# Optimization experiments

Hardware: AMD Instinct MI355X
Metric: run time of the kernel (lower is better)

## Reference

```python
import jax, jax.numpy as jnp
import numpy as np

B, S, D, H = 2, 2048, 1024, 16
HD = D // H  # head_dim = 64


def setup_inputs() -> dict:
    key = jax.random.key(0)
    ks = jax.random.split(key, 5)
    scale = 0.02
    x = jax.random.normal(ks[0], (B, S, D), dtype=jnp.float32)
    Wq = scale * jax.random.normal(ks[1], (H, D, HD), dtype=jnp.float32)
    Wk = scale * jax.random.normal(ks[2], (H, D, HD), dtype=jnp.float32)
    Wv = scale * jax.random.normal(ks[3], (H, D, HD), dtype=jnp.float32)
    Wo = scale * jax.random.normal(ks[4], (D, D), dtype=jnp.float32)
    bq = jnp.zeros((H, HD), dtype=jnp.float32)
    bk = jnp.zeros((H, HD), dtype=jnp.float32)
    bv = jnp.zeros((H, HD), dtype=jnp.float32)
    bo = jnp.zeros((D,), dtype=jnp.float32)
    return {"x": x, "Wq": Wq, "bq": bq, "Wk": Wk, "bk": bk,
            "Wv": Wv, "bv": bv, "Wo": Wo, "bo": bo}


def reference(x, Wq, bq, Wk, bk, Wv, bv, Wo, bo):
    # Per-head QKV projections (the torch module's per-head nn.Linear list,
    # vectorized over the head axis h). Dropout is identity (eval mode).
    q = jnp.einsum("bsd,hde->bhse", x, Wq) + bq[None, :, None, :]  # [B,H,S,HD]
    k = jnp.einsum("bsd,hde->bhse", x, Wk) + bk[None, :, None, :]
    v = jnp.einsum("bsd,hde->bhse", x, Wv) + bv[None, :, None, :]

    norm = jnp.asarray(np.sqrt(HD), dtype=x.dtype)
    scores = jnp.einsum("bhse,bhte->bhst", q, k) / norm  # [B,H,S,S]
    causal = jnp.tril(jnp.ones((S, S), dtype=bool))
    scores = jnp.where(causal[None, None], scores, jnp.asarray(-jnp.inf, dtype=scores.dtype))
    attn = jax.nn.softmax(scores, axis=-1)

    wv = jnp.einsum("bhst,bhte->bhse", attn, v)          # [B,H,S,HD]
    wv = jnp.transpose(wv, (0, 2, 1, 3)).reshape(B, S, D)  # concat heads on last dim
    out = wv @ Wo.T + bo                                   # output projection
    return out
```

## Files before the change

kernel.cpp:

```cpp
#include <hip/hip_runtime.h>


#define DD 1024
#define SS 2048
#define BB 2
#define HH 16
#define HD 64
#define QSCALE 0.18033688011112042f
#define LSTR 88

typedef __attribute__((ext_vector_type(8))) short short8;
typedef __attribute__((ext_vector_type(4))) float float4v;
typedef unsigned short ushort;
typedef unsigned int uint;

__device__ inline ushort f2bf(float f) {
    union { float f; uint i; } v; v.f = f;
    uint r = v.i + 0x7FFF + ((v.i >> 16) & 1);
    return (ushort)(r >> 16);
}
__device__ inline ushort f2bf_f(float f) {
    union { float f; uint i; } v; v.f = f;
    return (ushort)((v.i + 0x8000u) >> 16);
}

__device__ __forceinline__ void cp16(const ushort* g, ushort* l) {
    __builtin_amdgcn_global_load_lds((const __attribute__((address_space(1))) void*)g,
                                     (__attribute__((address_space(3))) void*)l,
                                     16, 0, 0);
}

__global__ __launch_bounds__(256) void cvt_all(const float* __restrict__ x,
                                               const float* __restrict__ Wo,
                                               ushort* __restrict__ xb,
                                               ushort* __restrict__ Wob) {
    const int NX4 = (BB * SS * DD) / 4;
    int i = blockIdx.x * 256 + threadIdx.x;
    const float* src; ushort* dst; int j;
    if (i < NX4) { src = x; dst = xb; j = i; }
    else         { src = Wo; dst = Wob; j = i - NX4; }
    float4 v = ((const float4*)src)[j];
    ushort o[4] = { f2bf(v.x), f2bf(v.y), f2bf(v.z), f2bf(v.w) };
    ((uint2*)dst)[j] = *(const uint2*)o;
}

__global__ __launch_bounds__(256) void transpose_w3(const float* __restrict__ Wq,
                                                    const float* __restrict__ Wk,
                                                    const float* __restrict__ Wv,
                                                    ushort* __restrict__ W3T) {
    __shared__ ushort T[64][65];
    int z = blockIdx.z;
    const float* W = z == 0 ? Wq : (z == 1 ? Wk : Wv);
    int h = blockIdx.y, d0 = blockIdx.x * 64;
    const float* Wh = W + h * DD * HD;
    ushort* Wt = W3T + ((size_t)z * HH + h) * HD * DD;
    int t = threadIdx.x;
    #pragma unroll
    for (int i = 0; i < 4; i++) {
        int idx = t + i * 256;
        int d = idx >> 4, e4 = (idx & 15) * 4;
        float4 v = *(const float4*)(Wh + (d0 + d) * HD + e4);
        T[d][e4 + 0] = f2bf(v.x); T[d][e4 + 1] = f2bf(v.y);
        T[d][e4 + 2] = f2bf(v.z); T[d][e4 + 3] = f2bf(v.w);
    }
    __syncthreads();
    #pragma unroll
    for (int i = 0; i < 2; i++) {
        int idx = t + i * 256;
        int e = idx >> 3, d8 = (idx & 7) * 8;
        ushort tmp[8];
        #pragma unroll
        for (int j = 0; j < 8; j++) tmp[j] = T[d8 + j][e];
        *(uint4*)(Wt + e * DD + d0 + d8) = *(uint4*)tmp;
    }
}

__global__ __launch_bounds__(256) void gemm_qkv(const ushort* __restrict__ xb,
                                                const ushort* __restrict__ W3T,
                                                const float* __restrict__ bq,
                                                const float* __restrict__ bk,
                                                const float* __restrict__ bv,
                                                ushort* __restrict__ qb,
                                                ushort* __restrict__ kb,
                                                ushort* __restrict__ vT) {
    __shared__ ushort Al[128 * 32];
    __shared__ ushort Bl[128 * 32];
    int z = blockIdx.z;
    const ushort* Wt   = W3T + (size_t)z * HH * HD * DD;
    const float*  bias = z == 0 ? bq : (z == 1 ? bk : bv);
    int m0 = blockIdx.x * 128, n0 = blockIdx.y * 128;
    int t = threadIdx.x, lane = t & 63, w = t >> 6;
    int wm = w & 1, wn = w >> 1;
    int qm = lane >> 4, lm = lane & 15;

    float4v acc[4][4] = {};
    for (int k0 = 0; k0 < DD; k0 += 32) {
        __syncthreads();
        #pragma unroll
        for (int r2 = 0; r2 < 2; r2++) {
            int c = t + r2 * 256;
            cp16(xb + (size_t)(m0 + (c >> 2)) * DD + k0 + (c & 3) * 8, Al + c * 8);
            cp16(Wt + (size_t)(n0 + (c >> 2)) * DD + k0 + (c & 3) * 8, Bl + c * 8);
        }
        __syncthreads();
        short8 a[4], b[4];
        #pragma unroll
        for (int i = 0; i < 4; i++)
            a[i] = *(const short8*)(Al + (wm * 64 + i * 16 + lm) * 32 + qm * 8);
        #pragma unroll
        for (int j = 0; j < 4; j++)
            b[j] = *(const short8*)(Bl + (wn * 64 + j * 16 + lm) * 32 + qm * 8);
        #pragma unroll
        for (int i = 0; i < 4; i++)
            #pragma unroll
            for (int j = 0; j < 4; j++)
                acc[i][j] = __builtin_amdgcn_mfma_f32_16x16x32_bf16(a[i], b[j], acc[i][j], 0, 0, 0);
    }
    if (z == 2) {
        #pragma unroll
        for (int j = 0; j < 4; j++) {
            int n = n0 + wn * 64 + j * 16 + lm;
            int h = n >> 6, e = n & 63;
            float bb = bias[n];
            #pragma unroll
            for (int i = 0; i < 4; i++) {
                int m = m0 + wm * 64 + i * 16 + qm * 4;
                int b_ = m >> 11, s = m & (SS - 1);
                ushort p4[4];
                #pragma unroll
                for (int r = 0; r < 4; r++) p4[r] = f2bf_f(acc[i][j][r] + bb);
                *(uint2*)(vT + ((size_t)(b_ * HH + h) * HD + e) * SS + s) = *(const uint2*)p4;
            }
        }
    } else {
        ushort* Out = z == 0 ? qb : kb;
        float sc = z == 0 ? QSCALE : 1.0f;
        #pragma unroll
        for (int j = 0; j < 4; j++) {
            int n = n0 + wn * 64 + j * 16 + lm;
            float bb = bias[n];
            #pragma unroll
            for (int i = 0; i < 4; i++)
                #pragma unroll
                for (int r = 0; r < 4; r++) {
                    int m = m0 + wm * 64 + i * 16 + qm * 4 + r;
                    Out[(size_t)m * DD + n] = f2bf_f((acc[i][j][r] + bb) * sc);
                }
        }
    }
}

__global__ __launch_bounds__(512) void attn(const ushort* __restrict__ Q,
                                            const ushort* __restrict__ K,
                                            const ushort* __restrict__ VT,
                                            ushort* __restrict__ O) {
    __shared__ ushort Ql[128][LSTR];
    __shared__ ushort Kl[2][64][LSTR];
    __shared__ ushort Vl[2][64][LSTR];
    __shared__ ushort Pl[8][16][LSTR];
    int px = blockIdx.x, bh = blockIdx.y;
    int b = bh >> 4, h = bh & 15;
    const ushort* Qp = Q + (size_t)b * SS * DD + h * HD;
    const ushort* Kp = K + (size_t)b * SS * DD + h * HD;
    const ushort* Vp = VT + (size_t)bh * HD * SS;
    int t = threadIdx.x, lane = t & 63, w = t >> 6;
    int qm = lane >> 4, lm = lane & 15;
    int row0 = t >> 3, colc = (t & 7) * 8;

    #pragma unroll
    for (int ph = 0; ph < 2; ph++) {
        int qt = ph ? 15 - px : px;
        int m0 = qt * 128;
        int njt = 2 * (qt + 1);
        __syncthreads();
        *(uint4*)(&Ql[row0][colc])      = *(const uint4*)(Qp + (size_t)(m0 + row0) * DD + colc);
        *(uint4*)(&Ql[row0 + 64][colc]) = *(const uint4*)(Qp + (size_t)(m0 + row0 + 64) * DD + colc);
        *(uint4*)(&Kl[0][row0][colc])   = *(const uint4*)(Kp + (size_t)row0 * DD + colc);
        *(uint4*)(&Vl[0][row0][colc])   = *(const uint4*)(Vp + (size_t)row0 * SS + colc);

        float4v o[4] = {};
        float mi = -__builtin_inff(), li = 0.f;
        int cur = 0;
        int qg = m0 + w * 16 + lm;

        for (int jt = 0; jt < njt; jt++) {
            __syncthreads();
            bool pre = jt + 1 < njt;
            uint4 pk, pv;
            if (pre) {
                int nn = (jt + 1) * 64;
                pk = *(const uint4*)(Kp + (size_t)(nn + row0) * DD + colc);
                pv = *(const uint4*)(Vp + (size_t)row0 * SS + nn + colc);
            }

            float4v s[4] = {};
            #pragma unroll
            for (int kc = 0; kc < 2; kc++) {
                short8 bq8 = *(const short8*)(&Ql[w * 16 + lm][kc * 32 + qm * 8]);
                #pragma unroll
                for (int j = 0; j < 4; j++) {
                    short8 ak = *(const short8*)(&Kl[cur][j * 16 + lm][kc * 32 + qm * 8]);
                    s[j] = __builtin_amdgcn_mfma_f32_16x16x32_bf16(ak, bq8, s[j], 0, 0, 0);
                }
            }
            if (jt >= 2 * qt) {
                #pragma unroll
                for (int j = 0; j < 4; j++)
                    #pragma unroll
                    for (int r = 0; r < 4; r++)
                        if (jt * 64 + j * 16 + qm * 4 + r > qg) s[j][r] = -__builtin_inff();
            }
            float mloc = s[0][0];
            #pragma unroll
            for (int j = 0; j < 4; j++)
                #pragma unroll
                for (int r = 0; r < 4; r++) mloc = fmaxf(mloc, s[j][r]);
            mloc = fmaxf(mloc, __shfl_xor(mloc, 16, 64));
            mloc = fmaxf(mloc, __shfl_xor(mloc, 32, 64));
            float mnew = fmaxf(mi, mloc);
            float sum = 0.f;
            #pragma unroll
            for (int j = 0; j < 4; j++)
                #pragma unroll
                for (int r = 0; r < 4; r++) {
                    float p = __builtin_amdgcn_exp2f(s[j][r] - mnew);
                    s[j][r] = p;
                    sum += p;
                }
            sum += __shfl_xor(sum, 16, 64);
            sum += __shfl_xor(sum, 32, 64);
            float alpha = __builtin_amdgcn_exp2f(mi - mnew);
            li = li * alpha + sum;
            mi = mnew;

            #pragma unroll
            for (int j = 0; j < 4; j++) {
                ushort p4[4];
                #pragma unroll
                for (int r = 0; r < 4; r++) p4[r] = f2bf_f(s[j][r]);
                *(uint2*)(&Pl[w][lm][j * 16 + qm * 4]) = *(const uint2*)p4;
            }
            #pragma unroll
            for (int r = 0; r < 4; r++) {
                float ar = __shfl(alpha, qm * 4 + r, 64);
                o[0][r] *= ar; o[1][r] *= ar; o[2][r] *= ar; o[3][r] *= ar;
            }
            asm volatile("s_waitcnt lgkmcnt(0)" ::: "memory");

            #pragma unroll
            for (int kc = 0; kc < 2; kc++) {
                short8 ap = *(const short8*)(&Pl[w][lm][kc * 32 + qm * 8]);
                #pragma unroll
                for (int jn = 0; jn < 4; jn++) {
                    short8 bv8 = *(const short8*)(&Vl[cur][jn * 16 + lm][kc * 32 + qm * 8]);
                    o[jn] = __builtin_amdgcn_mfma_f32_16x16x32_bf16(ap, bv8, o[jn], 0, 0, 0);
                }
            }
            if (pre) {
                *(uint4*)(&Kl[cur ^ 1][row0][colc]) = pk;
                *(uint4*)(&Vl[cur ^ 1][row0][colc]) = pv;
            }
            cur ^= 1;
        }
        float lr[4];
        #pragma unroll
        for (int r = 0; r < 4; r++) lr[r] = __shfl(li, qm * 4 + r, 64);
        #pragma unroll
        for (int jn = 0; jn < 4; jn++)
            #pragma unroll
            for (int r = 0; r < 4; r++) {
                int sg = m0 + w * 16 + qm * 4 + r;
                O[((size_t)b * SS + sg) * DD + h * HD + jn * 16 + lm] = f2bf_f(o[jn][r] / lr[r]);
            }
    }
}

__global__ __launch_bounds__(256) void gemm_out(const ushort* __restrict__ X,
                                                const ushort* __restrict__ Wob,
                                                const float* __restrict__ bo,
                                                float* __restrict__ Out) {
    __shared__ ushort Al[128 * 32];
    __shared__ ushort Bl[64 * 32];
    int m0 = blockIdx.x * 128, n0 = blockIdx.y * 64;
    int t = threadIdx.x, lane = t & 63, w = t >> 6;
    int wm = w & 1, wn = w >> 1;
    int qm = lane >> 4, lm = lane & 15;

    float4v acc[4][2] = {};
    for (int k0 = 0; k0 < DD; k0 += 32) {
        __syncthreads();
        #pragma unroll
        for (int r2 = 0; r2 < 2; r2++) {
            int c = t + r2 * 256;
            cp16(X + (size_t)(m0 + (c >> 2)) * DD + k0 + (c & 3) * 8, Al + c * 8);
        }
        cp16(Wob + (size_t)(n0 + (t >> 2)) * DD + k0 + (t & 3) * 8, Bl + t * 8);
        __syncthreads();
        short8 a[4], b[2];
        #pragma unroll
        for (int i = 0; i < 4; i++)
            a[i] = *(const short8*)(Al + (wm * 64 + i * 16 + lm) * 32 + qm * 8);
        #pragma unroll
        for (int j = 0; j < 2; j++)
            b[j] = *(const short8*)(Bl + (wn * 32 + j * 16 + lm) * 32 + qm * 8);
        #pragma unroll
        for (int i = 0; i < 4; i++)
            #pragma unroll
            for (int j = 0; j < 2; j++)
                acc[i][j] = __builtin_amdgcn_mfma_f32_16x16x32_bf16(a[i], b[j], acc[i][j], 0, 0, 0);
    }
    #pragma unroll
    for (int j = 0; j < 2; j++) {
        int n = n0 + wn * 32 + j * 16 + lm;
        float bb = bo[n];
        #pragma unroll
        for (int i = 0; i < 4; i++)
            #pragma unroll
            for (int r = 0; r < 4; r++) {
                int m = m0 + wm * 64 + i * 16 + qm * 4 + r;
                Out[(size_t)m * DD + n] = acc[i][j][r] + bb;
            }
    }
}

extern "C" void kernel_launch(void* const* d_in, const int* in_sizes, int n_in,
                              void* d_out, int out_size, void* d_ws, size_t ws_size,
                              hipStream_t stream) {
    const float* x   = (const float*)d_in[0];
    const float* Wq  = (const float*)d_in[1];
    const float* bq  = (const float*)d_in[2];
    const float* Wk  = (const float*)d_in[3];
    const float* bk  = (const float*)d_in[4];
    const float* Wv_ = (const float*)d_in[5];
    const float* bv  = (const float*)d_in[6];
    const float* Wo  = (const float*)d_in[7];
    const float* bo  = (const float*)d_in[8];
    float* out = (float*)d_out;

    ushort* xb  = (ushort*)d_ws;
    ushort* W3T = xb  + (size_t)BB * SS * DD;
    ushort* Wob = W3T + (size_t)3 * HH * HD * DD;
    ushort* qb  = Wob + (size_t)DD * DD;
    ushort* kb  = qb + (size_t)BB * SS * DD;
    ushort* vT  = kb + (size_t)BB * SS * DD;
    ushort* wvb = vT + (size_t)BB * SS * DD;

    cvt_all<<<dim3(5120), 256, 0, stream>>>(x, Wo, xb, Wob);
    transpose_w3<<<dim3(16, 16, 3), 256, 0, stream>>>(Wq, Wk, Wv_, W3T);
    gemm_qkv<<<dim3(32, 8, 3), 256, 0, stream>>>(xb, W3T, bq, bk, bv, qb, kb, vT);
    attn<<<dim3(8, 32), 512, 0, stream>>>(qb, kb, vT, wvb);
    gemm_out<<<dim3(32, 16), 256, 0, stream>>>(wvb, Wob, bo, out);
}
```

Baseline: 204.6 us.

## Split attention into one block per query tile, swap MFMA operands for vectorized stores

The attention kernel no longer pairs two query tiles per block. It launches one block per (tile, head), with the longest tiles scheduled first, and adds a launch_bounds occupancy hint. Q fragments are held in registers so the Q shared buffer can be reused for P, which removes the separate P buffer and cuts LDS per block. MFMA operands are swapped in attn, gemm_qkv (q/k paths) and gemm_out so each lane holds four consecutive columns. This allows packed 8-byte and 16-byte output stores and removes the per-row alpha and l shuffles. The cost is losing the balanced work pairing, which can leave causal load imbalance across blocks.

```diff
diff --git a/kernel.cpp b/kernel.cpp
--- a/kernel.cpp
+++ b/kernel.cpp
@@ -110,11 +110,19 @@
         #pragma unroll
         for (int j = 0; j < 4; j++)
             b[j] = *(const short8*)(Bl + (wn * 64 + j * 16 + lm) * 32 + qm * 8);
-        #pragma unroll
-        for (int i = 0; i < 4; i++)
-            #pragma unroll
-            for (int j = 0; j < 4; j++)
-                acc[i][j] = __builtin_amdgcn_mfma_f32_16x16x32_bf16(a[i], b[j], acc[i][j], 0, 0, 0);
+        if (z == 2) {
+            #pragma unroll
+            for (int i = 0; i < 4; i++)
+                #pragma unroll
+                for (int j = 0; j < 4; j++)
+                    acc[i][j] = __builtin_amdgcn_mfma_f32_16x16x32_bf16(a[i], b[j], acc[i][j], 0, 0, 0);
+        } else {
+            #pragma unroll
+            for (int i = 0; i < 4; i++)
+                #pragma unroll
+                for (int j = 0; j < 4; j++)
+                    acc[i][j] = __builtin_amdgcn_mfma_f32_16x16x32_bf16(b[j], a[i], acc[i][j], 0, 0, 0);
+        }
     }
     if (z == 2) {
         #pragma unroll
@@ -137,29 +145,34 @@
         float sc = z == 0 ? QSCALE : 1.0f;
         #pragma unroll
         for (int j = 0; j < 4; j++) {
-            int n = n0 + wn * 64 + j * 16 + lm;
-            float bb = bias[n];
-            #pragma unroll
-            for (int i = 0; i < 4; i++)
-                #pragma unroll
-                for (int r = 0; r < 4; r++) {
-                    int m = m0 + wm * 64 + i * 16 + qm * 4 + r;
-                    Out[(size_t)m * DD + n] = f2bf_f((acc[i][j][r] + bb) * sc);
-                }
-        }
-    }
-}
-
-__global__ __launch_bounds__(512) void attn(const ushort* __restrict__ Q,
-                                            const ushort* __restrict__ K,
-                                            const ushort* __restrict__ VT,
-                                            ushort* __restrict__ O) {
-    __shared__ ushort Ql[128][LSTR];
+            int nb = n0 + wn * 64 + j * 16 + qm * 4;
+            float4 b4 = *(const float4*)(bias + nb);
+            #pragma unroll
+            for (int i = 0; i < 4; i++) {
+                int m = m0 + wm * 64 + i * 16 + lm;
+                ushort p4[4];
+                p4[0] = f2bf_f((acc[i][j][0] + b4.x) * sc);
+                p4[1] = f2bf_f((acc[i][j][1] + b4.y) * sc);
+                p4[2] = f2bf_f((acc[i][j][2] + b4.z) * sc);
+                p4[3] = f2bf_f((acc[i][j][3] + b4.w) * sc);
+                *(uint2*)(Out + (size_t)m * DD + nb) = *(const uint2*)p4;
+            }
+        }
+    }
+}
+
+__global__ __launch_bounds__(512, 4) void attn(const ushort* __restrict__ Q,
+                                               const ushort* __restrict__ K,
+                                               const ushort* __restrict__ VT,
+                                               ushort* __restrict__ O) {
+    __shared__ ushort QP[128][LSTR];
     __shared__ ushort Kl[2][64][LSTR];
     __shared__ ushort Vl[2][64][LSTR];
-    __shared__ ushort Pl[8][16][LSTR];
-    int px = blockIdx.x, bh = blockIdx.y;
+    int bh = blockIdx.x, px = blockIdx.y;
+    int qt = 15 - px;
     int b = bh >> 4, h = bh & 15;
+    int m0 = qt * 128;
+    int njt = 2 * (qt + 1);
     const ushort* Qp = Q + (size_t)b * SS * DD + h * HD;
     const ushort* Kp = K + (size_t)b * SS * DD + h * HD;
     const ushort* Vp = VT + (size_t)bh * HD * SS;
@@ -167,111 +180,106 @@
     int qm = lane >> 4, lm = lane & 15;
     int row0 = t >> 3, colc = (t & 7) * 8;
 
-    #pragma unroll
-    for (int ph = 0; ph < 2; ph++) {
-        int qt = ph ? 15 - px : px;
-        int m0 = qt * 128;
-        int njt = 2 * (qt + 1);
-        __syncthreads();
-        *(uint4*)(&Ql[row0][colc])      = *(const uint4*)(Qp + (size_t)(m0 + row0) * DD + colc);
-        *(uint4*)(&Ql[row0 + 64][colc]) = *(const uint4*)(Qp + (size_t)(m0 + row0 + 64) * DD + colc);
-        *(uint4*)(&Kl[0][row0][colc])   = *(const uint4*)(Kp + (size_t)row0 * DD + colc);
-        *(uint4*)(&Vl[0][row0][colc])   = *(const uint4*)(Vp + (size_t)row0 * SS + colc);
-
-        float4v o[4] = {};
-        float mi = -__builtin_inff(), li = 0.f;
-        int cur = 0;
-        int qg = m0 + w * 16 + lm;
-
-        for (int jt = 0; jt < njt; jt++) {
-            __syncthreads();
-            bool pre = jt + 1 < njt;
-            uint4 pk, pv;
-            if (pre) {
-                int nn = (jt + 1) * 64;
-                pk = *(const uint4*)(Kp + (size_t)(nn + row0) * DD + colc);
-                pv = *(const uint4*)(Vp + (size_t)row0 * SS + nn + colc);
-            }
-
-            float4v s[4] = {};
-            #pragma unroll
-            for (int kc = 0; kc < 2; kc++) {
-                short8 bq8 = *(const short8*)(&Ql[w * 16 + lm][kc * 32 + qm * 8]);
-                #pragma unroll
-                for (int j = 0; j < 4; j++) {
-                    short8 ak = *(const short8*)(&Kl[cur][j * 16 + lm][kc * 32 + qm * 8]);
-                    s[j] = __builtin_amdgcn_mfma_f32_16x16x32_bf16(ak, bq8, s[j], 0, 0, 0);
-                }
-            }
-            if (jt >= 2 * qt) {
-                #pragma unroll
-                for (int j = 0; j < 4; j++)
-                    #pragma unroll
-                    for (int r = 0; r < 4; r++)
-                        if (jt * 64 + j * 16 + qm * 4 + r > qg) s[j][r] = -__builtin_inff();
-            }
-            float mloc = s[0][0];
+    *(uint4*)(&QP[row0][colc])      = *(const uint4*)(Qp + (size_t)(m0 + row0) * DD + colc);
+    *(uint4*)(&QP[row0 + 64][colc]) = *(const uint4*)(Qp + (size_t)(m0 + row0 + 64) * DD + colc);
+    *(uint4*)(&Kl[0][row0][colc])   = *(const uint4*)(Kp + (size_t)row0 * DD + colc);
+    *(uint4*)(&Vl[0][row0][colc])   = *(const uint4*)(Vp + (size_t)row0 * SS + colc);
+    __syncthreads();
+
+    short8 qf[2];
+    qf[0] = *(const short8*)(&QP[w * 16 + lm][qm * 8]);
+    qf[1] = *(const short8*)(&QP[w * 16 + lm][32 + qm * 8]);
+
+    float4v o[4] = {};
+    float mi = -__builtin_inff(), li = 0.f;
+    int cur = 0;
+    int qg = m0 + w * 16 + lm;
+
+    for (int jt = 0; jt < njt; jt++) {
+        if (jt) __syncthreads();
+        bool pre = jt + 1 < njt;
+        uint4 pk, pv;
+        if (pre) {
+            int nn = (jt + 1) * 64;
+            pk = *(const uint4*)(Kp + (size_t)(nn + row0) * DD + colc);
+            pv = *(const uint4*)(Vp + (size_t)row0 * SS + nn + colc);
+        }
+
+        float4v s[4] = {};
+        #pragma unroll
+        for (int kc = 0; kc < 2; kc++) {
+            #pragma unroll
+            for (int j = 0; j < 4; j++) {
+                short8 ak = *(const short8*)(&Kl[cur][j * 16 + lm][kc * 32 + qm * 8]);
+                s[j] = __builtin_amdgcn_mfma_f32_16x16x32_bf16(ak, qf[kc], s[j], 0, 0, 0);
+            }
+        }
+        if (jt >= 2 * qt) {
             #pragma unroll
             for (int j = 0; j < 4; j++)
                 #pragma unroll
-                for (int r = 0; r < 4; r++) mloc = fmaxf(mloc, s[j][r]);
-            mloc = fmaxf(mloc, __shfl_xor(mloc, 16, 64));
-            mloc = fmaxf(mloc, __shfl_xor(mloc, 32, 64));
-            float mnew = fmaxf(mi, mloc);
-            float sum = 0.f;
-            #pragma unroll
-            for (int j = 0; j < 4; j++)
-                #pragma unroll
-                for (int r = 0; r < 4; r++) {
-                    float p = __builtin_amdgcn_exp2f(s[j][r] - mnew);
-                    s[j][r] = p;
-                    sum += p;
-                }
-            sum += __shfl_xor(sum, 16, 64);
-            sum += __shfl_xor(sum, 32, 64);
-            float alpha = __builtin_amdgcn_exp2f(mi - mnew);
-            li = li * alpha + sum;
-            mi = mnew;
-
-            #pragma unroll
-            for (int j = 0; j < 4; j++) {
-                ushort p4[4];
-                #pragma unroll
-                for (int r = 0; r < 4; r++) p4[r] = f2bf_f(s[j][r]);
-                *(uint2*)(&Pl[w][lm][j * 16 + qm * 4]) = *(const uint2*)p4;
-            }
+                for (int r = 0; r < 4; r++)
+                    if (jt * 64 + j * 16 + qm * 4 + r > qg) s[j][r] = -__builtin_inff();
+        }
+        float mloc = s[0][0];
+        #pragma unroll
+        for (int j = 0; j < 4; j++)
+            #pragma unroll
+            for (int r = 0; r < 4; r++) mloc = fmaxf(mloc, s[j][r]);
+        mloc = fmaxf(mloc, __shfl_xor(mloc, 16, 64));
+        mloc = fmaxf(mloc, __shfl_xor(mloc, 32, 64));
+        float mnew = fmaxf(mi, mloc);
+        float sum = 0.f;
+        #pragma unroll
+        for (int j = 0; j < 4; j++)
             #pragma unroll
             for (int r = 0; r < 4; r++) {
-                float ar = __shfl(alpha, qm * 4 + r, 64);
-                o[0][r] *= ar; o[1][r] *= ar; o[2][r] *= ar; o[3][r] *= ar;
-            }
-            asm volatile("s_waitcnt lgkmcnt(0)" ::: "memory");
-
-            #pragma unroll
-            for (int kc = 0; kc < 2; kc++) {
-                short8 ap = *(const short8*)(&Pl[w][lm][kc * 32 + qm * 8]);
-                #pragma unroll
-                for (int jn = 0; jn < 4; jn++) {
-                    short8 bv8 = *(const short8*)(&Vl[cur][jn * 16 + lm][kc * 32 + qm * 8]);
-                    o[jn] = __builtin_amdgcn_mfma_f32_16x16x32_bf16(ap, bv8, o[jn], 0, 0, 0);
-                }
-            }
-            if (pre) {
-                *(uint4*)(&Kl[cur ^ 1][row0][colc]) = pk;
-                *(uint4*)(&Vl[cur ^ 1][row0][colc]) = pv;
-            }
-            cur ^= 1;
-        }
-        float lr[4];
-        #pragma unroll
-        for (int r = 0; r < 4; r++) lr[r] = __shfl(li, qm * 4 + r, 64);
+                float p = __builtin_amdgcn_exp2f(s[j][r] - mnew);
+                s[j][r] = p;
+                sum += p;
+            }
+        sum += __shfl_xor(sum, 16, 64);
+        sum += __shfl_xor(sum, 32, 64);
+        float alpha = __builtin_amdgcn_exp2f(mi - mnew);
+        li = li * alpha + sum;
+        mi = mnew;
+
+        #pragma unroll
+        for (int j = 0; j < 4; j++) {
+            ushort p4[4];
+            #pragma unroll
+            for (int r = 0; r < 4; r++) p4[r] = f2bf_f(s[j][r]);
+            *(uint2*)(&QP[w * 16 + lm][j * 16 + qm * 4]) = *(const uint2*)p4;
+        }
         #pragma unroll
         for (int jn = 0; jn < 4; jn++)
             #pragma unroll
-            for (int r = 0; r < 4; r++) {
-                int sg = m0 + w * 16 + qm * 4 + r;
-                O[((size_t)b * SS + sg) * DD + h * HD + jn * 16 + lm] = f2bf_f(o[jn][r] / lr[r]);
-            }
+            for (int r = 0; r < 4; r++) o[jn][r] *= alpha;
+        asm volatile("s_waitcnt lgkmcnt(0)" ::: "memory");
+
+        #pragma unroll
+        for (int kc = 0; kc < 2; kc++) {
+            short8 ap = *(const short8*)(&QP[w * 16 + lm][kc * 32 + qm * 8]);
+            #pragma unroll
+            for (int jn = 0; jn < 4; jn++) {
+                short8 av = *(const short8*)(&Vl[cur][jn * 16 + lm][kc * 32 + qm * 8]);
+                o[jn] = __builtin_amdgcn_mfma_f32_16x16x32_bf16(av, ap, o[jn], 0, 0, 0);
+            }
+        }
+        if (pre) {
+            *(uint4*)(&Kl[cur ^ 1][row0][colc]) = pk;
+            *(uint4*)(&Vl[cur ^ 1][row0][colc]) = pv;
+        }
+        cur ^= 1;
+    }
+    float inv = 1.f / li;
+    ushort* Ob = O + ((size_t)b * SS + qg) * DD + h * HD;
+    #pragma unroll
+    for (int jn = 0; jn < 4; jn++) {
+        ushort p4[4];
+        #pragma unroll
+        for (int r = 0; r < 4; r++) p4[r] = f2bf_f(o[jn][r] * inv);
+        *(uint2*)(Ob + jn * 16 + qm * 4) = *(const uint2*)p4;
     }
 }
 
@@ -307,19 +315,22 @@
         for (int i = 0; i < 4; i++)
             #pragma unroll
             for (int j = 0; j < 2; j++)
-                acc[i][j] = __builtin_amdgcn_mfma_f32_16x16x32_bf16(a[i], b[j], acc[i][j], 0, 0, 0);
+                acc[i][j] = __builtin_amdgcn_mfma_f32_16x16x32_bf16(b[j], a[i], acc[i][j], 0, 0, 0);
     }
     #pragma unroll
     for (int j = 0; j < 2; j++) {
-        int n = n0 + wn * 32 + j * 16 + lm;
-        float bb = bo[n];
-        #pragma unroll
-        for (int i = 0; i < 4; i++)
-            #pragma unroll
-            for (int r = 0; r < 4; r++) {
-                int m = m0 + wm * 64 + i * 16 + qm * 4 + r;
-                Out[(size_t)m * DD + n] = acc[i][j][r] + bb;
-            }
+        int nb = n0 + wn * 32 + j * 16 + qm * 4;
+        float4 b4 = *(const float4*)(bo + nb);
+        #pragma unroll
+        for (int i = 0; i < 4; i++) {
+            int m = m0 + wm * 64 + i * 16 + lm;
+            float4 st;
+            st.x = acc[i][j][0] + b4.x;
+            st.y = acc[i][j][1] + b4.y;
+            st.z = acc[i][j][2] + b4.z;
+            st.w = acc[i][j][3] + b4.w;
+            *(float4*)(Out + (size_t)m * DD + nb) = st;
+        }
     }
 }
 
@@ -348,6 +359,6 @@
     cvt_all<<<dim3(5120), 256, 0, stream>>>(x, Wo, xb, Wob);
     transpose_w3<<<dim3(16, 16, 3), 256, 0, stream>>>(Wq, Wk, Wv_, W3T);
     gemm_qkv<<<dim3(32, 8, 3), 256, 0, stream>>>(xb, W3T, bq, bk, bv, qb, kb, vT);
-    attn<<<dim3(8, 32), 512, 0, stream>>>(qb, kb, vT, wvb);
+    attn<<<dim3(32, 16), 512, 0, stream>>>(qb, kb, vT, wvb);
     gemm_out<<<dim3(32, 16), 256, 0, stream>>>(wvb, Wob, bo, out);
 }
```

Measured after the change: 205.6 us. Within noise of the previous version (+0.5%).
